# Kernel tuning notes

Measured on AMD Instinct MI355X. Metric: run time of the kernel, lower is better.

## Reference

```python
import jax, jax.numpy as jnp
import numpy as np

B, T, S, N, MOTOR, CLASSES = 256, 2048, 32, 19, 1, 10
UNFOLDS = 6      # ode_unfolds in LTCCell
EPS = 1e-8


def setup_inputs() -> dict:
    key = jax.random.key(0)
    ks = jax.random.split(key, 20)
    d = {}
    d["x"] = jax.random.normal(ks[0], (B, T, S), jnp.float32)
    d["input_w"] = jax.random.uniform(ks[1], (S,), jnp.float32)
    d["input_b"] = jax.random.normal(ks[2], (S,), jnp.float32)
    d["sensory_mu"] = jax.random.uniform(ks[3], (S, N), jnp.float32)
    d["sensory_sigma"] = jax.random.uniform(ks[4], (S, N), jnp.float32)
    d["sensory_w"] = jax.random.uniform(ks[5], (S, N), jnp.float32)
    d["sensory_erev"] = jax.random.normal(ks[6], (S, N), jnp.float32)
    d["mu"] = jax.random.uniform(ks[7], (N, N), jnp.float32)
    d["sigma"] = jax.random.uniform(ks[8], (N, N), jnp.float32)
    d["w"] = jax.random.uniform(ks[9], (N, N), jnp.float32)
    d["erev"] = jax.random.normal(ks[10], (N, N), jnp.float32)
    d["gleak"] = jax.random.uniform(ks[11], (N,), jnp.float32)
    d["vleak"] = jax.random.normal(ks[12], (N,), jnp.float32)
    d["cm"] = jax.random.uniform(ks[13], (N,), jnp.float32)
    d["output_w"] = jax.random.uniform(ks[14], (MOTOR,), jnp.float32)
    d["output_b"] = jax.random.normal(ks[15], (MOTOR,), jnp.float32)
    d["fc_w"] = jax.random.normal(ks[16], (CLASSES, MOTOR * T), jnp.float32) * 0.02
    d["fc_b"] = jax.random.normal(ks[17], (CLASSES,), jnp.float32)
    d["sensory_mask"] = jax.random.randint(ks[18], (S, N), 0, 2, jnp.int32)
    d["mask"] = jax.random.randint(ks[19], (N, N), 0, 2, jnp.int32)
    return d


def reference(x, input_w, input_b, sensory_mu, sensory_sigma, sensory_w,
              sensory_erev, mu, sigma, w, erev, gleak, vleak, cm,
              output_w, output_b, fc_w, fc_b, sensory_mask, mask):
    smask = sensory_mask.astype(x.dtype)   # (S, N) sensory->state wiring
    m = mask.astype(x.dtype)               # (N, N) state->state wiring
    bsz = x.shape[0]
    # map_inputs: affine per-sensory-channel, then time-major for scan
    xt = (x * input_w + input_b).transpose(1, 0, 2)   # (T, B, S)
    cm_t = cm * UNFOLDS                               # cm / (elapsed_time / unfolds)

    def step(v, inp):
        # sensory synapse activation: (B, S, N)
        sa = sensory_w * jax.nn.sigmoid(sensory_sigma * (inp[:, :, None] - sensory_mu)) * smask
        w_num_s = jnp.sum(sa * sensory_erev, axis=1)  # (B, N)
        w_den_s = jnp.sum(sa, axis=1)                 # (B, N)
        for _ in range(UNFOLDS):
            # recurrent synapse activation: (B, N_pre, N_post)
            wa = w * jax.nn.sigmoid(sigma * (v[:, :, None] - mu)) * m
            w_num = jnp.sum(wa * erev, axis=1) + w_num_s
            w_den = jnp.sum(wa, axis=1) + w_den_s
            v = (cm_t * v + gleak * vleak + w_num) / (cm_t + gleak + w_den + EPS)
        out = v[:, :MOTOR] * output_w + output_b      # map_outputs (motor neurons first)
        return v, out

    v0 = jnp.zeros((bsz, N), x.dtype)
    _, outs = jax.lax.scan(step, v0, xt)              # outs: (T, B, MOTOR)
    flat = outs.transpose(1, 0, 2).reshape(bsz, -1)   # (B, MOTOR*T)
    return flat @ fc_w.T + fc_b                       # (B, CLASSES)
```

## Files before the change

### kernel.cpp

```cpp
#include <hip/hip_runtime.h>

#define BB 256
#define TT 2048
#define SS 32
#define NN 19
#define NCLASS 10
#define NUNFOLD 6
#define EPSV 1e-8f
#define LOG2E 1.4426950408889634f
#define CH 128
#define NCH (TT / CH)
#define SROW 39

template <int CTRL>
__device__ __forceinline__ float dpp_shl(float x)
{
    return __int_as_float(__builtin_amdgcn_update_dpp(
        0, __float_as_int(x), CTRL, 0xf, 0xf, true));
}

__device__ __forceinline__ float bperm(int addr4, float v)
{
    return __int_as_float(__builtin_amdgcn_ds_bpermute(addr4, __float_as_int(v)));
}

__device__ __forceinline__ int lead_lane(int i)
{
    int rw = i / 5;
    return 16 * rw + 3 * (i % 5) + (rw >= 2 ? 1 : 0);
}

template <int KU>
__device__ __forceinline__ void fused_loop(
    int tid, int lane, int wid, int b, int jc,
    const float (&sg2)[8], const float (&sb2)[8],
    const float (&Aa)[8], const float (&Wm)[8], const int (&src4)[8],
    float cmt, float glvl, float cgl, float ow0, float ob0,
    const float* __restrict__ x,
    const float4* __restrict__ pq,
    float* __restrict__ sbuf,
    float* __restrict__ obuf)
{
    float v = 0.f;
    for (int c = 0; c <= NCH; c++) {
        if (wid != 0) {
            if (c < NCH) {
                float* sb = sbuf + (c & 1) * (CH * SROW);
                const float* xb = x + ((long)b * TT + (long)c * CH) * SS;
                for (int tl = tid - 64; tl < CH; tl += 192) {
                    const float4* xr4 = (const float4*)(xb + tl * SS);
                    float xs[SS];
#pragma unroll
                    for (int q = 0; q < SS / 4; q++) {
                        float4 v4 = xr4[q];
                        xs[4 * q + 0] = v4.x; xs[4 * q + 1] = v4.y;
                        xs[4 * q + 2] = v4.z; xs[4 * q + 3] = v4.w;
                    }
                    float* srow = sb + tl * SROW;
                    for (int j = 0; j < NN; j++) {
                        const float4* pp = pq + j * SS;
                        float num = 0.f, den = 0.f;
#pragma unroll 4
                        for (int s = 0; s < SS; s += 2) {
                            float4 c0 = pp[s];
                            float4 c1 = pp[s + 1];
                            float e0 = __builtin_amdgcn_exp2f(fmaf(c0.y, xs[s], c0.x));
                            float e1 = __builtin_amdgcn_exp2f(fmaf(c1.y, xs[s + 1], c1.x));
                            float t0v = 1.0f + e0, t1v = 1.0f + e1;
                            float rD = __builtin_amdgcn_rcpf(t0v * t1v);
                            num = fmaf(fmaf(c0.w, t1v, c1.w * t0v), rD, num);
                            den = fmaf(fmaf(c0.z, t1v, c1.z * t0v), rD, den);
                        }
                        srow[j]      = num;
                        srow[NN + j] = den;
                    }
                }
            }
        } else if (c > 0) {
            const float* sb = sbuf + ((c - 1) & 1) * (CH * SROW);
            float sn = sb[jc], sd = sb[NN + jc];
            int tbase = (c - 1) * CH;
            for (int tl = 0; tl < CH; tl++) {
                float sn_nx = sn, sd_nx = sd;
                if (tl + 1 < CH) {
                    sn_nx = sb[(tl + 1) * SROW + jc];
                    sd_nx = sb[(tl + 1) * SROW + NN + jc];
                }
                float nbase = glvl + sn, dbase = cgl + sd;
#pragma unroll
                for (int u = 0; u < NUNFOLD; u++) {
                    float vi[KU];
#pragma unroll
                    for (int k = 0; k < KU; k++) vi[k] = bperm(src4[k], v);
                    float n = fmaf(cmt, v, nbase);
                    float ev[KU];
#pragma unroll
                    for (int k = 0; k < KU; k++)
                        ev[k] = __builtin_amdgcn_exp2f(fmaf(sg2[k], vi[k], sb2[k]));
                    float pn = 0.f, pd = 0.f;
                    constexpr int NP = KU / 2;
#pragma unroll
                    for (int p = 0; p < NP; p++) {
                        float t0v = 1.0f + ev[2 * p];
                        float t1v = 1.0f + ev[2 * p + 1];
                        float rD  = __builtin_amdgcn_rcpf(t0v * t1v);
                        pn = fmaf(fmaf(Aa[2 * p], t1v, Aa[2 * p + 1] * t0v), rD, pn);
                        pd = fmaf(fmaf(Wm[2 * p], t1v, Wm[2 * p + 1] * t0v), rD, pd);
                    }
                    if (KU & 1) {
                        float s1 = __builtin_amdgcn_rcpf(1.0f + ev[KU - 1]);
                        pn = fmaf(Aa[KU - 1], s1, pn);
                        pd = fmaf(Wm[KU - 1], s1, pd);
                    }
                    pn = pn + dpp_shl<0x101>(pn) + dpp_shl<0x102>(pn);
                    pd = pd + dpp_shl<0x101>(pd) + dpp_shl<0x102>(pd);
                    v = (n + pn) * __builtin_amdgcn_rcpf(dbase + pd);
                }
                if (lane == 0) obuf[tbase + tl] = fmaf(v, ow0, ob0);
                sn = sn_nx; sd = sd_nx;
            }
        }
        __syncthreads();
    }
}

__global__ void __launch_bounds__(256, 1)
ltc_fused_kernel(const float* __restrict__ x,
                 const float* __restrict__ iw,  const float* __restrict__ ib,
                 const float* __restrict__ smu, const float* __restrict__ ssig,
                 const float* __restrict__ sw,  const float* __restrict__ serev,
                 const int* __restrict__ smask,
                 const float* __restrict__ mu,  const float* __restrict__ sigma,
                 const float* __restrict__ w,   const float* __restrict__ erev,
                 const int* __restrict__ mask,
                 const float* __restrict__ gleak, const float* __restrict__ vleak,
                 const float* __restrict__ cm,
                 const float* __restrict__ ow,  const float* __restrict__ ob,
                 const float* __restrict__ fcw, const float* __restrict__ fcb,
                 float* __restrict__ out)
{
    __shared__ float4 pq[SS * NN];
    __shared__ float  sbuf[2 * CH * SROW];
    __shared__ float  obuf[TT];
    __shared__ float  red[4 * NCLASS];

    int tid  = threadIdx.x;
    int b    = blockIdx.x;
    int lane = tid & 63;
    int wid  = tid >> 6;

    for (int idx = tid; idx < SS * NN; idx += 256) {
        int j = idx >> 5;
        int s = idx & 31;
        int src = s * NN + j;
        float sg = ssig[src] * LOG2E;
        float P  = sg * smu[src] - sg * ib[s];
        float Qn = -sg * iw[s];
        float wm = sw[src] * (float)smask[src];
        pq[idx] = make_float4(P, Qn, wm, wm * serev[src]);
    }

    int row  = lane >> 4;
    int pos  = lane & 15;
    int off  = (row >= 2) ? 1 : 0;
    int posr = pos - off;
    int jq   = (posr < 0) ? 5 : posr / 3;
    int rr   = (posr < 0) ? 0 : posr - 3 * jq;
    int j    = row * 5 + jq;
    bool pad = (jq >= 5) || (j >= NN);
    int jc   = pad ? 0 : j;
    int r    = pad ? 0 : rr;

    float sg2[8], sb2[8], Aa[8], Wm[8];
    int src4[8];
    int used = 0;
#pragma unroll
    for (int s = 0; s < 8; s++) {
        int target = 3 * s + r;
        int ii = -1, a = 0;
        for (int i = 0; i < NN; i++) {
            if (mask[i * NN + jc] != 0) {
                if (a == target) ii = i;
                a++;
            }
        }
        bool ok = (ii >= 0) && !pad;
        int iu  = ok ? ii : 0;
        int idx = iu * NN + jc;
        float sgv = sigma[idx];
        float wmm = ok ? w[idx] : 0.f;
        sg2[s] = ok ? (-LOG2E * sgv) : 0.f;
        sb2[s] = ok ? (LOG2E * sgv * mu[idx]) : 0.f;
        Aa[s]  = wmm * erev[idx];
        Wm[s]  = wmm;
        src4[s] = lead_lane(iu) << 2;
        if (ok) used = s + 1;
    }
    int km = used;
#pragma unroll
    for (int o = 1; o < 64; o <<= 1) {
        int other = __shfl_xor(km, o, 64);
        km = km > other ? km : other;
    }

    float cmt   = cm[jc] * (float)NUNFOLD;
    float gl    = gleak[jc];
    float glvl  = gl * vleak[jc];
    float cgl   = cmt + gl + EPSV;
    float ow0 = ow[0], ob0 = ob[0];

    __syncthreads();

    if (km <= 3)
        fused_loop<3>(tid, lane, wid, b, jc, sg2, sb2, Aa, Wm, src4,
                      cmt, glvl, cgl, ow0, ob0, x, pq, sbuf, obuf);
    else if (km == 4)
        fused_loop<4>(tid, lane, wid, b, jc, sg2, sb2, Aa, Wm, src4,
                      cmt, glvl, cgl, ow0, ob0, x, pq, sbuf, obuf);
    else if (km == 5)
        fused_loop<5>(tid, lane, wid, b, jc, sg2, sb2, Aa, Wm, src4,
                      cmt, glvl, cgl, ow0, ob0, x, pq, sbuf, obuf);
    else if (km == 6)
        fused_loop<6>(tid, lane, wid, b, jc, sg2, sb2, Aa, Wm, src4,
                      cmt, glvl, cgl, ow0, ob0, x, pq, sbuf, obuf);
    else
        fused_loop<7>(tid, lane, wid, b, jc, sg2, sb2, Aa, Wm, src4,
                      cmt, glvl, cgl, ow0, ob0, x, pq, sbuf, obuf);

    float acc[NCLASS];
#pragma unroll
    for (int c = 0; c < NCLASS; c++) acc[c] = 0.f;
    for (int t = tid; t < TT; t += 256) {
        float ov = obuf[t];
#pragma unroll
        for (int c = 0; c < NCLASS; c++)
            acc[c] = fmaf(ov, fcw[c * TT + t], acc[c]);
    }
#pragma unroll
    for (int c = 0; c < NCLASS; c++) {
#pragma unroll
        for (int o2 = 32; o2 > 0; o2 >>= 1)
            acc[c] += __shfl_down(acc[c], o2, 64);
    }
    if (lane == 0) {
#pragma unroll
        for (int c = 0; c < NCLASS; c++) red[wid * NCLASS + c] = acc[c];
    }
    __syncthreads();
    if (tid < NCLASS)
        out[b * NCLASS + tid] = red[tid] + red[NCLASS + tid]
                              + red[2 * NCLASS + tid] + red[3 * NCLASS + tid]
                              + fcb[tid];
}

extern "C" void kernel_launch(void* const* d_in, const int* in_sizes, int n_in,
                              void* d_out, int out_size, void* d_ws, size_t ws_size,
                              hipStream_t stream)
{
    const float* x     = (const float*)d_in[0];
    const float* iw    = (const float*)d_in[1];
    const float* ib    = (const float*)d_in[2];
    const float* smu   = (const float*)d_in[3];
    const float* ssig  = (const float*)d_in[4];
    const float* sw    = (const float*)d_in[5];
    const float* serev = (const float*)d_in[6];
    const float* mu    = (const float*)d_in[7];
    const float* sigma = (const float*)d_in[8];
    const float* w     = (const float*)d_in[9];
    const float* erev  = (const float*)d_in[10];
    const float* gleak = (const float*)d_in[11];
    const float* vleak = (const float*)d_in[12];
    const float* cm    = (const float*)d_in[13];
    const float* ow    = (const float*)d_in[14];
    const float* ob    = (const float*)d_in[15];
    const float* fcw   = (const float*)d_in[16];
    const float* fcb   = (const float*)d_in[17];
    const int* smask   = (const int*)d_in[18];
    const int* mask    = (const int*)d_in[19];
    float* out = (float*)d_out;

    ltc_fused_kernel<<<BB, 256, 0, stream>>>(x, iw, ib, smu, ssig, sw, serev,
                                             smask, mu, sigma, w, erev, mask,
                                             gleak, vleak, cm, ow, ob,
                                             fcw, fcb, out);
}
```

Before: 1.789 ms.

## Broadcast state via readlane to SGPRs instead of ds_bpermute gather

Replaces the per-unfold ds_bpermute gather of presynaptic voltages with 19 readlane broadcasts into uniform registers, and changes the lane layout to a fixed 3-lane-per-neuron split in which each lane handles presynaptic indices i = 3q+h. Per-lane coefficients cA/cB/cC select the relevant scalar, which removes the mask-compaction logic and the km template dispatch. The goal is to take LDS-permute latency off the serial recurrence chain. In exchange every lane now always evaluates 7 exp/rcp terms, even for unused synapses, and the readlanes are serialized scalar operations.

```diff
diff --git a/kernel.cpp b/kernel.cpp
--- a/kernel.cpp
+++ b/kernel.cpp
@@ -11,6 +11,7 @@
 #define CH 128
 #define NCH (TT / CH)
 #define SROW 39
+#define NU 7
 
 template <int CTRL>
 __device__ __forceinline__ float dpp_shl(float x)
@@ -19,22 +20,15 @@
         0, __float_as_int(x), CTRL, 0xf, 0xf, true));
 }
 
-__device__ __forceinline__ float bperm(int addr4, float v)
-{
-    return __int_as_float(__builtin_amdgcn_ds_bpermute(addr4, __float_as_int(v)));
-}
-
-__device__ __forceinline__ int lead_lane(int i)
-{
-    int rw = i / 5;
-    return 16 * rw + 3 * (i % 5) + (rw >= 2 ? 1 : 0);
-}
-
-template <int KU>
+__device__ __forceinline__ float rdlane(float v, int l)
+{
+    return __int_as_float(__builtin_amdgcn_readlane(__float_as_int(v), l));
+}
+
 __device__ __forceinline__ void fused_loop(
     int tid, int lane, int wid, int b, int jc,
-    const float (&sg2)[8], const float (&sb2)[8],
-    const float (&Aa)[8], const float (&Wm)[8], const int (&src4)[8],
+    const float (&cA)[NU], const float (&cB)[NU], const float (&cC)[NU],
+    const float (&sb2)[NU], const float (&Aa)[NU], const float (&Wm)[NU],
     float cmt, float glvl, float cgl, float ow0, float ob0,
     const float* __restrict__ x,
     const float4* __restrict__ pq,
@@ -42,6 +36,10 @@
     float* __restrict__ obuf)
 {
     float v = 0.f;
+    float vS[NN];
+#pragma unroll
+    for (int i0 = 0; i0 < NN; i0++) vS[i0] = 0.f;
+
     for (int c = 0; c <= NCH; c++) {
         if (wid != 0) {
             if (c < NCH) {
@@ -89,32 +87,34 @@
                 float nbase = glvl + sn, dbase = cgl + sd;
 #pragma unroll
                 for (int u = 0; u < NUNFOLD; u++) {
-                    float vi[KU];
-#pragma unroll
-                    for (int k = 0; k < KU; k++) vi[k] = bperm(src4[k], v);
-                    float n = fmaf(cmt, v, nbase);
-                    float ev[KU];
-#pragma unroll
-                    for (int k = 0; k < KU; k++)
-                        ev[k] = __builtin_amdgcn_exp2f(fmaf(sg2[k], vi[k], sb2[k]));
+                    float tv[NU];
+#pragma unroll
+                    for (int q = 0; q < NU; q++) {
+                        float t = fmaf(vS[3 * q], cA[q], sb2[q]);
+                        if (3 * q + 1 < NN) t = fmaf(vS[3 * q + 1], cB[q], t);
+                        if (3 * q + 2 < NN) t = fmaf(vS[3 * q + 2], cC[q], t);
+                        tv[q] = 1.0f + __builtin_amdgcn_exp2f(t);
+                    }
                     float pn = 0.f, pd = 0.f;
-                    constexpr int NP = KU / 2;
-#pragma unroll
-                    for (int p = 0; p < NP; p++) {
-                        float t0v = 1.0f + ev[2 * p];
-                        float t1v = 1.0f + ev[2 * p + 1];
+#pragma unroll
+                    for (int p = 0; p < NU / 2; p++) {
+                        float t0v = tv[2 * p], t1v = tv[2 * p + 1];
                         float rD  = __builtin_amdgcn_rcpf(t0v * t1v);
                         pn = fmaf(fmaf(Aa[2 * p], t1v, Aa[2 * p + 1] * t0v), rD, pn);
                         pd = fmaf(fmaf(Wm[2 * p], t1v, Wm[2 * p + 1] * t0v), rD, pd);
                     }
-                    if (KU & 1) {
-                        float s1 = __builtin_amdgcn_rcpf(1.0f + ev[KU - 1]);
-                        pn = fmaf(Aa[KU - 1], s1, pn);
-                        pd = fmaf(Wm[KU - 1], s1, pd);
+                    {
+                        float s1 = __builtin_amdgcn_rcpf(tv[NU - 1]);
+                        pn = fmaf(Aa[NU - 1], s1, pn);
+                        pd = fmaf(Wm[NU - 1], s1, pd);
                     }
                     pn = pn + dpp_shl<0x101>(pn) + dpp_shl<0x102>(pn);
                     pd = pd + dpp_shl<0x101>(pd) + dpp_shl<0x102>(pd);
+                    float n = fmaf(cmt, v, nbase);
                     v = (n + pn) * __builtin_amdgcn_rcpf(dbase + pd);
+#pragma unroll
+                    for (int jj = 0; jj < NN; jj++)
+                        vS[jj] = rdlane(v, (jj / 5) * 16 + (jj % 5) * 3);
                 }
                 if (lane == 0) obuf[tbase + tl] = fmaf(v, ow0, ob0);
                 sn = sn_nx; sd = sd_nx;
@@ -160,47 +160,29 @@
         pq[idx] = make_float4(P, Qn, wm, wm * serev[src]);
     }
 
-    int row  = lane >> 4;
-    int pos  = lane & 15;
-    int off  = (row >= 2) ? 1 : 0;
-    int posr = pos - off;
-    int jq   = (posr < 0) ? 5 : posr / 3;
-    int rr   = (posr < 0) ? 0 : posr - 3 * jq;
-    int j    = row * 5 + jq;
-    bool pad = (jq >= 5) || (j >= NN);
-    int jc   = pad ? 0 : j;
-    int r    = pad ? 0 : rr;
-
-    float sg2[8], sb2[8], Aa[8], Wm[8];
-    int src4[8];
-    int used = 0;
-#pragma unroll
-    for (int s = 0; s < 8; s++) {
-        int target = 3 * s + r;
-        int ii = -1, a = 0;
-        for (int i = 0; i < NN; i++) {
-            if (mask[i * NN + jc] != 0) {
-                if (a == target) ii = i;
-                a++;
-            }
-        }
-        bool ok = (ii >= 0) && !pad;
-        int iu  = ok ? ii : 0;
-        int idx = iu * NN + jc;
-        float sgv = sigma[idx];
+    int row = lane >> 4;
+    int pos = lane & 15;
+    int m   = pos / 3;
+    int h   = pos - 3 * m;
+    int j   = row * 5 + m;
+    bool pad = (pos >= 15) || (j >= NN);
+    int jc  = pad ? 0 : j;
+
+    float cA[NU], cB[NU], cC[NU], sb2[NU], Aa[NU], Wm[NU];
+#pragma unroll
+    for (int q = 0; q < NU; q++) {
+        int i = 3 * q + h;
+        bool ok = !pad && (i < NN) && (mask[i * NN + jc] != 0);
+        int idx = (ok ? i : 0) * NN + jc;
+        float sgl = sigma[idx] * LOG2E;
+        float sg2 = ok ? -sgl : 0.f;
+        sb2[q] = ok ? sgl * mu[idx] : 0.f;
         float wmm = ok ? w[idx] : 0.f;
-        sg2[s] = ok ? (-LOG2E * sgv) : 0.f;
-        sb2[s] = ok ? (LOG2E * sgv * mu[idx]) : 0.f;
-        Aa[s]  = wmm * erev[idx];
-        Wm[s]  = wmm;
-        src4[s] = lead_lane(iu) << 2;
-        if (ok) used = s + 1;
-    }
-    int km = used;
-#pragma unroll
-    for (int o = 1; o < 64; o <<= 1) {
-        int other = __shfl_xor(km, o, 64);
-        km = km > other ? km : other;
+        Aa[q] = wmm * erev[idx];
+        Wm[q] = wmm;
+        cA[q] = (h == 0) ? sg2 : 0.f;
+        cB[q] = (h == 1) ? sg2 : 0.f;
+        cC[q] = (h == 2) ? sg2 : 0.f;
     }
 
     float cmt   = cm[jc] * (float)NUNFOLD;
@@ -211,21 +193,8 @@
 
     __syncthreads();
 
-    if (km <= 3)
-        fused_loop<3>(tid, lane, wid, b, jc, sg2, sb2, Aa, Wm, src4,
-                      cmt, glvl, cgl, ow0, ob0, x, pq, sbuf, obuf);
-    else if (km == 4)
-        fused_loop<4>(tid, lane, wid, b, jc, sg2, sb2, Aa, Wm, src4,
-                      cmt, glvl, cgl, ow0, ob0, x, pq, sbuf, obuf);
-    else if (km == 5)
-        fused_loop<5>(tid, lane, wid, b, jc, sg2, sb2, Aa, Wm, src4,
-                      cmt, glvl, cgl, ow0, ob0, x, pq, sbuf, obuf);
-    else if (km == 6)
-        fused_loop<6>(tid, lane, wid, b, jc, sg2, sb2, Aa, Wm, src4,
-                      cmt, glvl, cgl, ow0, ob0, x, pq, sbuf, obuf);
-    else
-        fused_loop<7>(tid, lane, wid, b, jc, sg2, sb2, Aa, Wm, src4,
-                      cmt, glvl, cgl, ow0, ob0, x, pq, sbuf, obuf);
+    fused_loop(tid, lane, wid, b, jc, cA, cB, cC, sb2, Aa, Wm,
+               cmt, glvl, cgl, ow0, ob0, x, pq, sbuf, obuf);
 
     float acc[NCLASS];
 #pragma unroll
```

Measured after the change: 2.469 ms. +38.0%, slower.
